# Kernel optimization log

Hardware: AMD Instinct MI355X
Metric: run time of the kernel (lower is better)

## Reference

```python
import jax, jax.numpy as jnp
import numpy as np

# Model dims (match init_kwargs)
D_MODEL = 512
NUM_EXPERTS = 8
TOP_K = 2
FFN_MULT = 2
HIDDEN = FFN_MULT * D_MODEL
BATCH, SEQ = 4, 2048


def setup_inputs() -> dict:
    key = jax.random.key(0)
    k_x, k_g, k_bg, k_w1, k_w3, k_w2 = jax.random.split(key, 6)
    sd = 1.0 / np.sqrt(D_MODEL).astype(np.float32)
    sh = 1.0 / np.sqrt(HIDDEN).astype(np.float32)
    return {
        "x": jax.random.normal(k_x, (BATCH, SEQ, D_MODEL), dtype=jnp.float32),
        # gate: nn.Linear(d_model, num_experts) with bias
        "Wg": jax.random.normal(k_g, (D_MODEL, NUM_EXPERTS), dtype=jnp.float32) * sd,
        "bg": jax.random.normal(k_bg, (NUM_EXPERTS,), dtype=jnp.float32) * 0.01,
        # stacked per-expert SwiGLU FFN params (no bias, LLaMA-style)
        "W1": jax.random.normal(k_w1, (NUM_EXPERTS, D_MODEL, HIDDEN), dtype=jnp.float32) * sd,
        "W3": jax.random.normal(k_w3, (NUM_EXPERTS, D_MODEL, HIDDEN), dtype=jnp.float32) * sd,
        "W2": jax.random.normal(k_w2, (NUM_EXPERTS, HIDDEN, D_MODEL), dtype=jnp.float32) * sh,
    }


def reference(x, Wg, bg, W1, W3, W2):
    B, S, D = x.shape
    E = Wg.shape[1]
    xt = x.reshape(-1, D)                        # [T, D], T = B*S
    T = xt.shape[0]

    # Router: top-k over experts, softmax over the k selected logits
    logits = xt @ Wg + bg                        # [T, E]
    top_vals, top_idx = jax.lax.top_k(logits, TOP_K)  # [T, K]
    top_probs = jax.nn.softmax(top_vals, axis=-1)     # [T, K]

    # Dense per-(token, expert) combine weight; zero where expert not selected.
    # top-k indices are distinct per token so scatter-add == scatter-set.
    gate_w = jnp.zeros((T, E), dtype=xt.dtype).at[
        jnp.arange(T)[:, None], top_idx
    ].add(top_probs)                              # [T, E]

    # Loop over experts (fixed, small), accumulate weighted expert outputs.
    def body(y, expert):
        w1, w3, w2, g = expert                   # g: [T]
        h = jax.nn.silu(xt @ w1) * (xt @ w3)     # [T, H]
        return y + g[:, None] * (h @ w2), None

    y0 = jnp.zeros_like(xt)
    y, _ = jax.lax.scan(body, y0, (W1, W3, W2, gate_w.T))
    return y.reshape(B, S, D)
```

## Files before the change

### kernel.cpp

```cpp
#include <hip/hip_runtime.h>
#include <hip/hip_bf16.h>

#define TOKENS 8192
#define DM 512
#define NE 8
#define HID 1024
#define NSLOT (TOKENS * 2)
#define NB 32

#define BM 128
#define BN 64
#define BK 64
#define MAXTILE 136

typedef __bf16 bf16x8 __attribute__((ext_vector_type(8)));
typedef float floatx4 __attribute__((ext_vector_type(4)));
typedef unsigned short u16x8 __attribute__((ext_vector_type(8)));

__device__ __forceinline__ unsigned short f2bf(float f) {
    union { float f; unsigned u; } c; c.f = f;
    unsigned u = c.u;
    u += 0x7fffu + ((u >> 16) & 1u);
    return (unsigned short)(u >> 16);
}

__device__ __forceinline__ void load16_lds(const void* g, void* l) {
    __builtin_amdgcn_global_load_lds(
        (const __attribute__((address_space(1))) unsigned int*)g,
        (__attribute__((address_space(3))) unsigned int*)l, 16, 0, 0);
}

__global__ void init_kernel(float* __restrict__ y) {
    const size_t n4 = (size_t)TOKENS * DM / 4;
    float4* y4 = (float4*)y;
    for (size_t i = (size_t)blockIdx.x * blockDim.x + threadIdx.x; i < n4;
         i += (size_t)gridDim.x * blockDim.x)
        y4[i] = make_float4(0.f, 0.f, 0.f, 0.f);
}

__global__ void cvt_transpose_kernel(const float* __restrict__ src, unsigned short* __restrict__ dst,
                                     int K, int N) {
    __shared__ float tile[32][33];
    const int tk = K >> 5, tn = N >> 5;
    int b = blockIdx.x;
    int e = b / (tk * tn);
    int rem = b % (tk * tn);
    int kt = rem / tn, nt = rem % tn;
    int tx = threadIdx.x & 31, ty = threadIdx.x >> 5;
    const float* s = src + ((size_t)e * K + kt * 32) * N + nt * 32;
    #pragma unroll
    for (int i = 0; i < 32; i += 8)
        tile[ty + i][tx] = s[(size_t)(ty + i) * N + tx];
    __syncthreads();
    unsigned short* d = dst + ((size_t)e * N + nt * 32) * K + kt * 32;
    #pragma unroll
    for (int i = 0; i < 32; i += 8)
        d[(size_t)(ty + i) * K + tx] = f2bf(tile[tx][ty + i]);
}

__global__ void router_kernel(const float* __restrict__ x, const float* __restrict__ Wg,
                              const float* __restrict__ bg,
                              int* __restrict__ top_idx, float* __restrict__ top_p,
                              unsigned short* __restrict__ xb) {
    int lane = threadIdx.x & 63, wave = threadIdx.x >> 6;
    int t = blockIdx.x * 4 + wave;
    float acc[NE];
    #pragma unroll
    for (int e = 0; e < NE; e++) acc[e] = 0.f;
    const float* xr = x + (size_t)t * DM;
    unsigned short* xbr = xb + (size_t)t * DM;
    #pragma unroll
    for (int j = 0; j < 8; j++) {
        int d = lane + j * 64;
        float xv = xr[d];
        xbr[d] = f2bf(xv);
        const float4* wr = (const float4*)(Wg + (size_t)d * NE);
        float4 w0 = wr[0], w1 = wr[1];
        acc[0] += xv * w0.x; acc[1] += xv * w0.y; acc[2] += xv * w0.z; acc[3] += xv * w0.w;
        acc[4] += xv * w1.x; acc[5] += xv * w1.y; acc[6] += xv * w1.z; acc[7] += xv * w1.w;
    }
    #pragma unroll
    for (int e = 0; e < NE; e++) {
        float v = acc[e];
        #pragma unroll
        for (int off = 32; off > 0; off >>= 1) v += __shfl_down(v, off, 64);
        acc[e] = v;
    }
    if (lane == 0) {
        float best = -1e30f, second = -1e30f;
        int bi = 0, si = 0;
        #pragma unroll
        for (int e = 0; e < NE; e++) {
            float v = acc[e] + bg[e];
            if (v > best) { second = best; si = bi; best = v; bi = e; }
            else if (v > second) { second = v; si = e; }
        }
        float ex = __expf(second - best);
        float inv = 1.f / (1.f + ex);
        top_idx[t * 2] = bi;  top_idx[t * 2 + 1] = si;
        top_p[t * 2] = inv;   top_p[t * 2 + 1] = ex * inv;
    }
}

__global__ void hist_kernel(const int* __restrict__ top_idx, int* __restrict__ block_hist) {
    __shared__ int h[NE];
    int b = blockIdx.x, tid = threadIdx.x;
    if (tid < NE) h[tid] = 0;
    __syncthreads();
    int t = b * 256 + tid;
    atomicAdd(&h[top_idx[t * 2]], 1);
    atomicAdd(&h[top_idx[t * 2 + 1]], 1);
    __syncthreads();
    if (tid < NE) block_hist[b * NE + tid] = h[tid];
}

__global__ void prefix_kernel(const int* __restrict__ block_hist, int* __restrict__ counts,
                              int* __restrict__ offsets, int* __restrict__ bases) {
    int e = threadIdx.x;
    if (e < NE) {
        int run = 0;
        for (int b = 0; b < NB; b++) { bases[b * NE + e] = run; run += block_hist[b * NE + e]; }
        counts[e] = run;
    }
    __syncthreads();
    if (e == 0) {
        int s = 0;
        for (int ee = 0; ee < NE; ee++) { offsets[ee] = s; s += counts[ee]; }
    }
    __syncthreads();
    if (e < NE) {
        int off = offsets[e];
        for (int b = 0; b < NB; b++) bases[b * NE + e] += off;
    }
}

__global__ void build_kernel(const int* __restrict__ top_idx, const float* __restrict__ top_p,
                             const int* __restrict__ bases,
                             int* __restrict__ rows, float* __restrict__ gates,
                             int* __restrict__ slot_of) {
    __shared__ int cur[NE];
    int b = blockIdx.x, tid = threadIdx.x;
    if (tid < NE) cur[tid] = bases[b * NE + tid];
    __syncthreads();
    int t = b * 256 + tid;
    #pragma unroll
    for (int k = 0; k < 2; k++) {
        int e = top_idx[t * 2 + k];
        int slot = atomicAdd(&cur[e], 1);
        rows[slot] = t;
        gates[slot] = top_p[t * 2 + k];
        slot_of[t * 2 + k] = slot;
    }
}

__device__ __forceinline__ bool tile_lookup(const int* counts, const int* offsets, int gy,
                                            int& e, int& mt, int& cnt, int& off) {
    int bacc = 0;
    #pragma unroll
    for (int ee = 0; ee < NE; ee++) {
        int c = counts[ee];
        int ntl = (c + BM - 1) >> 7;
        if (gy < bacc + ntl) { e = ee; mt = gy - bacc; cnt = c; off = offsets[ee]; return true; }
        bacc += ntl;
    }
    return false;
}

__global__ __launch_bounds__(256) void gemm1_kernel(
    const unsigned short* __restrict__ xb,
    const unsigned short* __restrict__ w1t,
    const unsigned short* __restrict__ w3t,
    unsigned short* __restrict__ Hb,
    const int* __restrict__ rows, const int* __restrict__ counts,
    const int* __restrict__ offsets) {
    const int nt = blockIdx.x;
    int e, mt, cnt, off;
    if (!tile_lookup(counts, offsets, blockIdx.y, e, mt, cnt, off)) return;

    __shared__ unsigned short As[2][BM * BK];
    __shared__ unsigned short B1s[2][BN * BK];
    __shared__ unsigned short B3s[2][BN * BK];

    const int tid = threadIdx.x;
    const int lane = tid & 63, wave = tid >> 6;
    const int lrow8 = lane >> 3;
    const int lchunk = (lane & 7) ^ lrow8;

    const unsigned short* a_g[4];
    #pragma unroll
    for (int i = 0; i < 4; i++) {
        int r = (wave * 4 + i) * 8 + lrow8;
        int gr = mt * BM + r;
        int tok = rows[off + (gr < cnt ? gr : 0)];
        a_g[i] = xb + (size_t)tok * DM + lchunk * 8;
    }
    const unsigned short* b1_g[2]; const unsigned short* b3_g[2];
    #pragma unroll
    for (int i = 0; i < 2; i++) {
        int r = (wave * 2 + i) * 8 + lrow8;
        b1_g[i] = w1t + ((size_t)e * HID + nt * BN + r) * DM + lchunk * 8;
        b3_g[i] = w3t + ((size_t)e * HID + nt * BN + r) * DM + lchunk * 8;
    }

    const int l15 = lane & 15, quad = lane >> 4;
    const int sw = l15 & 7;

    floatx4 acc1[2][4], acc3[2][4];
    #pragma unroll
    for (int i = 0; i < 2; i++)
        #pragma unroll
        for (int j = 0; j < 4; j++) {
            acc1[i][j] = (floatx4){0.f, 0.f, 0.f, 0.f};
            acc3[i][j] = (floatx4){0.f, 0.f, 0.f, 0.f};
        }

    auto stage = [&](int k0, int b) {
        #pragma unroll
        for (int i = 0; i < 4; i++) load16_lds(a_g[i] + k0, &As[b][(wave * 4 + i) * 512]);
        #pragma unroll
        for (int i = 0; i < 2; i++) {
            load16_lds(b1_g[i] + k0, &B1s[b][(wave * 2 + i) * 512]);
            load16_lds(b3_g[i] + k0, &B3s[b][(wave * 2 + i) * 512]);
        }
    };
    auto compute = [&](int b) {
        #pragma unroll
        for (int kk = 0; kk < 2; kk++) {
            const int qc = kk * 4 + quad;
            const int ch = (qc ^ sw) << 3;
            bf16x8 af[2], b1f[4], b3f[4];
            #pragma unroll
            for (int mi = 0; mi < 2; mi++)
                af[mi] = *(const bf16x8*)(&As[b][(wave * 32 + mi * 16 + l15) * 64 + ch]);
            #pragma unroll
            for (int ni = 0; ni < 4; ni++) {
                b1f[ni] = *(const bf16x8*)(&B1s[b][(ni * 16 + l15) * 64 + ch]);
                b3f[ni] = *(const bf16x8*)(&B3s[b][(ni * 16 + l15) * 64 + ch]);
            }
            #pragma unroll
            for (int mi = 0; mi < 2; mi++)
                #pragma unroll
                for (int ni = 0; ni < 4; ni++) {
                    acc1[mi][ni] = __builtin_amdgcn_mfma_f32_16x16x32_bf16(af[mi], b1f[ni], acc1[mi][ni], 0, 0, 0);
                    acc3[mi][ni] = __builtin_amdgcn_mfma_f32_16x16x32_bf16(af[mi], b3f[ni], acc3[mi][ni], 0, 0, 0);
                }
        }
    };

    const int NI = DM / BK;
    stage(0, 0);
    #pragma unroll
    for (int i = 0; i < NI; i += 2) {
        __syncthreads();
        if (i + 1 < NI) stage((i + 1) * BK, 1);
        compute(0);
        __syncthreads();
        if (i + 2 < NI) stage((i + 2) * BK, 0);
        compute(1);
    }
    #pragma unroll
    for (int mi = 0; mi < 2; mi++) {
        #pragma unroll
        for (int r = 0; r < 4; r++) {
            int mloc = wave * 32 + mi * 16 + quad * 4 + r;
            int gi = mt * BM + mloc;
            if (gi < cnt) {
                size_t rowbase = (size_t)(off + gi) * HID + nt * BN;
                #pragma unroll
                for (int ni = 0; ni < 4; ni++) {
                    float z1 = acc1[mi][ni][r];
                    float z3 = acc3[mi][ni][r];
                    float h = (z1 / (1.f + __expf(-z1))) * z3;
                    Hb[rowbase + ni * 16 + l15] = f2bf(h);
                }
            }
        }
    }
}

__global__ __launch_bounds__(256) void gemm2_kernel(
    const unsigned short* __restrict__ Hb,
    const unsigned short* __restrict__ w2t,
    float* __restrict__ P,
    float* __restrict__ y,
    const int* __restrict__ rows, const float* __restrict__ gates,
    const int* __restrict__ counts, const int* __restrict__ offsets) {
    const int nt = blockIdx.x;
    int e, mt, cnt, off;
    if (!tile_lookup(counts, offsets, blockIdx.y, e, mt, cnt, off)) return;

    __shared__ unsigned short As[2][BM * BK];
    __shared__ unsigned short Bs[2][BN * BK];

    const int tid = threadIdx.x;
    const int lane = tid & 63, wave = tid >> 6;
    const int lrow8 = lane >> 3;
    const int lchunk = (lane & 7) ^ lrow8;

    const unsigned short* a_g[4];
    #pragma unroll
    for (int i = 0; i < 4; i++) {
        int r = (wave * 4 + i) * 8 + lrow8;
        int sl = off + mt * BM + r;
        if (sl >= NSLOT) sl = NSLOT - 1;
        a_g[i] = Hb + (size_t)sl * HID + lchunk * 8;
    }
    const unsigned short* b_g[2];
    #pragma unroll
    for (int i = 0; i < 2; i++) {
        int r = (wave * 2 + i) * 8 + lrow8;
        b_g[i] = w2t + ((size_t)e * DM + nt * BN + r) * HID + lchunk * 8;
    }

    const int l15 = lane & 15, quad = lane >> 4;
    const int sw = l15 & 7;

    floatx4 acc[2][4];
    #pragma unroll
    for (int i = 0; i < 2; i++)
        #pragma unroll
        for (int j = 0; j < 4; j++) acc[i][j] = (floatx4){0.f, 0.f, 0.f, 0.f};

    auto stage = [&](int k0, int b) {
        #pragma unroll
        for (int i = 0; i < 4; i++) load16_lds(a_g[i] + k0, &As[b][(wave * 4 + i) * 512]);
        #pragma unroll
        for (int i = 0; i < 2; i++) load16_lds(b_g[i] + k0, &Bs[b][(wave * 2 + i) * 512]);
    };
    auto compute = [&](int b) {
        #pragma unroll
        for (int kk = 0; kk < 2; kk++) {
            const int qc = kk * 4 + quad;
            const int ch = (qc ^ sw) << 3;
            bf16x8 af[2], bf[4];
            #pragma unroll
            for (int mi = 0; mi < 2; mi++)
                af[mi] = *(const bf16x8*)(&As[b][(wave * 32 + mi * 16 + l15) * 64 + ch]);
            #pragma unroll
            for (int ni = 0; ni < 4; ni++)
                bf[ni] = *(const bf16x8*)(&Bs[b][(ni * 16 + l15) * 64 + ch]);
            #pragma unroll
            for (int mi = 0; mi < 2; mi++)
                #pragma unroll
                for (int ni = 0; ni < 4; ni++)
                    acc[mi][ni] = __builtin_amdgcn_mfma_f32_16x16x32_bf16(af[mi], bf[ni], acc[mi][ni], 0, 0, 0);
        }
    };

    const int NI = HID / BK;
    stage(0, 0);
    #pragma unroll
    for (int i = 0; i < NI; i += 2) {
        __syncthreads();
        if (i + 1 < NI) stage((i + 1) * BK, 1);
        compute(0);
        __syncthreads();
        if (i + 2 < NI) stage((i + 2) * BK, 0);
        compute(1);
    }
    const bool direct = (P == nullptr);
    #pragma unroll
    for (int mi = 0; mi < 2; mi++) {
        #pragma unroll
        for (int r = 0; r < 4; r++) {
            int mloc = wave * 32 + mi * 16 + quad * 4 + r;
            int gi = mt * BM + mloc;
            if (gi < cnt) {
                int slot = off + gi;
                float g = gates[slot];
                #pragma unroll
                for (int ni = 0; ni < 4; ni++) {
                    int col = nt * BN + ni * 16 + l15;
                    float v = g * acc[mi][ni][r];
                    if (direct) {
                        int tokr = rows[slot];
                        atomicAdd(&y[(size_t)tokr * DM + col], v);
                    } else {
                        P[(size_t)slot * DM + col] = v;
                    }
                }
            }
        }
    }
}

__global__ void combine_kernel(const float* __restrict__ P, const int* __restrict__ slot_of,
                               float* __restrict__ y) {
    int i = blockIdx.x * blockDim.x + threadIdx.x;
    int t = i / (DM / 4);
    int c4 = i % (DM / 4);
    int s0 = slot_of[t * 2], s1 = slot_of[t * 2 + 1];
    float4 a = ((const float4*)P)[(size_t)s0 * (DM / 4) + c4];
    float4 b = ((const float4*)P)[(size_t)s1 * (DM / 4) + c4];
    float4 o;
    o.x = a.x + b.x;
    o.y = a.y + b.y;
    o.z = a.z + b.z;
    o.w = a.w + b.w;
    ((float4*)y)[i] = o;
}

extern "C" void kernel_launch(void* const* d_in, const int* in_sizes, int n_in,
                              void* d_out, int out_size, void* d_ws, size_t ws_size,
                              hipStream_t stream) {
    (void)in_sizes; (void)n_in; (void)out_size;
    const float* x  = (const float*)d_in[0];
    const float* Wg = (const float*)d_in[1];
    const float* bg = (const float*)d_in[2];
    const float* W1 = (const float*)d_in[3];
    const float* W3 = (const float*)d_in[4];
    const float* W2 = (const float*)d_in[5];
    float* y = (float*)d_out;

    char* p = (char*)d_ws;
    auto carve = [&](size_t bytes) -> char* {
        char* r = p;
        p += (bytes + 255) & ~(size_t)255;
        return r;
    };
    unsigned short* xb   = (unsigned short*)carve((size_t)TOKENS * DM * 2);
    unsigned short* w1t  = (unsigned short*)carve((size_t)NE * DM * HID * 2);
    unsigned short* w3t  = (unsigned short*)carve((size_t)NE * DM * HID * 2);
    unsigned short* w2t  = (unsigned short*)carve((size_t)NE * HID * DM * 2);
    unsigned short* Hb   = (unsigned short*)carve((size_t)NSLOT * HID * 2);
    int*   rows    = (int*)carve(NSLOT * 4);
    float* gates   = (float*)carve(NSLOT * 4);
    int*   slot_of = (int*)carve(NSLOT * 4);
    int*   tidx    = (int*)carve((size_t)TOKENS * 2 * 4);
    float* tp      = (float*)carve((size_t)TOKENS * 2 * 4);
    int*   counts  = (int*)carve(256);
    int*   offsets = (int*)carve(256);
    int*   bhist   = (int*)carve((size_t)NB * NE * 4);
    int*   bases   = (int*)carve((size_t)NB * NE * 4);
    size_t base_need = (size_t)(p - (char*)d_ws);
    const size_t PBYTES = (size_t)NSLOT * DM * 4;
    float* P = nullptr;
    if (ws_size >= base_need + PBYTES) P = (float*)carve(PBYTES);

    if (P == nullptr)
        init_kernel<<<dim3(1024), dim3(256), 0, stream>>>(y);
    router_kernel<<<dim3(TOKENS / 4), dim3(256), 0, stream>>>(x, Wg, bg, tidx, tp, xb);
    cvt_transpose_kernel<<<dim3(NE * (DM / 32) * (HID / 32)), dim3(256), 0, stream>>>(W1, w1t, DM, HID);
    cvt_transpose_kernel<<<dim3(NE * (DM / 32) * (HID / 32)), dim3(256), 0, stream>>>(W3, w3t, DM, HID);
    cvt_transpose_kernel<<<dim3(NE * (HID / 32) * (DM / 32)), dim3(256), 0, stream>>>(W2, w2t, HID, DM);
    hist_kernel<<<dim3(NB), dim3(256), 0, stream>>>(tidx, bhist);
    prefix_kernel<<<dim3(1), dim3(64), 0, stream>>>(bhist, counts, offsets, bases);
    build_kernel<<<dim3(NB), dim3(256), 0, stream>>>(tidx, tp, bases, rows, gates, slot_of);
    gemm1_kernel<<<dim3(HID / BN, MAXTILE, 1), dim3(256), 0, stream>>>(xb, w1t, w3t, Hb, rows, counts, offsets);
    gemm2_kernel<<<dim3(DM / BN, MAXTILE, 1), dim3(256), 0, stream>>>(Hb, w2t, P, y, rows, gates, counts, offsets);
    if (P != nullptr)
        combine_kernel<<<dim3((TOKENS * DM / 4) / 256), dim3(256), 0, stream>>>(P, slot_of, y);
}
```

Measured before the change: 241.1 us.

## Enlarge GEMM tiles to 2D wave layout, halve BK, merge weight-convert launches

Both expert GEMMs move from 1D row-split waves to a 2x2 (or 4x2) wave grid with 64x64 per-wave sub-tiles. This uses bigger block tiles (128x128 for gemm1, 256x128 with 512 threads for gemm2) and BK 32 with a new LDS swizzle. The goal is more operand reuse per LDS load and fewer global loads per FLOP. The three weight convert-transpose launches are merged into one 2D-grid launch to cut launch overhead. Larger accumulator arrays raise register pressure, and fewer, larger tiles mean more padding waste on partial expert tiles.

```diff
diff --git a/kernel.cpp b/kernel.cpp
--- a/kernel.cpp
+++ b/kernel.cpp
@@ -8,10 +8,13 @@
 #define NSLOT (TOKENS * 2)
 #define NB 32
 
-#define BM 128
-#define BN 64
-#define BK 64
-#define MAXTILE 136
+#define BK 32
+#define BM1 128
+#define BN1 128
+#define MAXTILE1 136
+#define BM2 256
+#define BN2 128
+#define MAXTILE2 72
 
 typedef __bf16 bf16x8 __attribute__((ext_vector_type(8)));
 typedef float floatx4 __attribute__((ext_vector_type(4)));
@@ -38,9 +41,15 @@
         y4[i] = make_float4(0.f, 0.f, 0.f, 0.f);
 }
 
-__global__ void cvt_transpose_kernel(const float* __restrict__ src, unsigned short* __restrict__ dst,
-                                     int K, int N) {
+__global__ void cvt_transpose_kernel(const float* __restrict__ W1, const float* __restrict__ W3,
+                                     const float* __restrict__ W2,
+                                     unsigned short* __restrict__ w1t, unsigned short* __restrict__ w3t,
+                                     unsigned short* __restrict__ w2t) {
     __shared__ float tile[32][33];
+    const float* src; unsigned short* dst; int K, N;
+    if (blockIdx.y == 0)      { src = W1; dst = w1t; K = DM;  N = HID; }
+    else if (blockIdx.y == 1) { src = W3; dst = w3t; K = DM;  N = HID; }
+    else                      { src = W2; dst = w2t; K = HID; N = DM;  }
     const int tk = K >> 5, tn = N >> 5;
     int b = blockIdx.x;
     int e = b / (tk * tn);
@@ -154,19 +163,19 @@
 }
 
 __device__ __forceinline__ bool tile_lookup(const int* counts, const int* offsets, int gy,
-                                            int& e, int& mt, int& cnt, int& off) {
+                                            int bmshift, int& e, int& mt, int& cnt, int& off) {
     int bacc = 0;
     #pragma unroll
     for (int ee = 0; ee < NE; ee++) {
         int c = counts[ee];
-        int ntl = (c + BM - 1) >> 7;
+        int ntl = (c + (1 << bmshift) - 1) >> bmshift;
         if (gy < bacc + ntl) { e = ee; mt = gy - bacc; cnt = c; off = offsets[ee]; return true; }
         bacc += ntl;
     }
     return false;
 }
 
-__global__ __launch_bounds__(256) void gemm1_kernel(
+__global__ __launch_bounds__(256, 2) void gemm1_kernel(
     const unsigned short* __restrict__ xb,
     const unsigned short* __restrict__ w1t,
     const unsigned short* __restrict__ w3t,
@@ -175,39 +184,40 @@
     const int* __restrict__ offsets) {
     const int nt = blockIdx.x;
     int e, mt, cnt, off;
-    if (!tile_lookup(counts, offsets, blockIdx.y, e, mt, cnt, off)) return;
-
-    __shared__ unsigned short As[2][BM * BK];
-    __shared__ unsigned short B1s[2][BN * BK];
-    __shared__ unsigned short B3s[2][BN * BK];
+    if (!tile_lookup(counts, offsets, blockIdx.y, 7, e, mt, cnt, off)) return;
+
+    __shared__ unsigned short As[2][BM1 * BK];
+    __shared__ unsigned short B1s[2][BN1 * BK];
+    __shared__ unsigned short B3s[2][BN1 * BK];
 
     const int tid = threadIdx.x;
     const int lane = tid & 63, wave = tid >> 6;
-    const int lrow8 = lane >> 3;
-    const int lchunk = (lane & 7) ^ lrow8;
-
-    const unsigned short* a_g[4];
-    #pragma unroll
-    for (int i = 0; i < 4; i++) {
-        int r = (wave * 4 + i) * 8 + lrow8;
-        int gr = mt * BM + r;
+    const int lr = lane >> 2;
+    const int lc = (lane & 3) ^ ((lane >> 3) & 3);
+
+    const unsigned short* a_g[2];
+    #pragma unroll
+    for (int i = 0; i < 2; i++) {
+        int r = wave * 32 + i * 16 + lr;
+        int gr = mt * BM1 + r;
         int tok = rows[off + (gr < cnt ? gr : 0)];
-        a_g[i] = xb + (size_t)tok * DM + lchunk * 8;
+        a_g[i] = xb + (size_t)tok * DM + lc * 8;
     }
     const unsigned short* b1_g[2]; const unsigned short* b3_g[2];
     #pragma unroll
     for (int i = 0; i < 2; i++) {
-        int r = (wave * 2 + i) * 8 + lrow8;
-        b1_g[i] = w1t + ((size_t)e * HID + nt * BN + r) * DM + lchunk * 8;
-        b3_g[i] = w3t + ((size_t)e * HID + nt * BN + r) * DM + lchunk * 8;
+        int r = wave * 32 + i * 16 + lr;
+        b1_g[i] = w1t + ((size_t)e * HID + nt * BN1 + r) * DM + lc * 8;
+        b3_g[i] = w3t + ((size_t)e * HID + nt * BN1 + r) * DM + lc * 8;
     }
 
     const int l15 = lane & 15, quad = lane >> 4;
-    const int sw = l15 & 7;
-
-    floatx4 acc1[2][4], acc3[2][4];
-    #pragma unroll
-    for (int i = 0; i < 2; i++)
+    const int rsw = (l15 >> 1) & 3;
+    const int m0 = (wave >> 1) * 64, n0 = (wave & 1) * 64;
+
+    floatx4 acc1[4][4], acc3[4][4];
+    #pragma unroll
+    for (int i = 0; i < 4; i++)
         #pragma unroll
         for (int j = 0; j < 4; j++) {
             acc1[i][j] = (floatx4){0.f, 0.f, 0.f, 0.f};
@@ -216,40 +226,34 @@
 
     auto stage = [&](int k0, int b) {
         #pragma unroll
-        for (int i = 0; i < 4; i++) load16_lds(a_g[i] + k0, &As[b][(wave * 4 + i) * 512]);
-        #pragma unroll
         for (int i = 0; i < 2; i++) {
-            load16_lds(b1_g[i] + k0, &B1s[b][(wave * 2 + i) * 512]);
-            load16_lds(b3_g[i] + k0, &B3s[b][(wave * 2 + i) * 512]);
+            load16_lds(a_g[i] + k0, &As[b][(wave * 32 + i * 16) * BK]);
+            load16_lds(b1_g[i] + k0, &B1s[b][(wave * 32 + i * 16) * BK]);
+            load16_lds(b3_g[i] + k0, &B3s[b][(wave * 32 + i * 16) * BK]);
         }
     };
     auto compute = [&](int b) {
-        #pragma unroll
-        for (int kk = 0; kk < 2; kk++) {
-            const int qc = kk * 4 + quad;
-            const int ch = (qc ^ sw) << 3;
-            bf16x8 af[2], b1f[4], b3f[4];
-            #pragma unroll
-            for (int mi = 0; mi < 2; mi++)
-                af[mi] = *(const bf16x8*)(&As[b][(wave * 32 + mi * 16 + l15) * 64 + ch]);
+        const int ch = ((quad ^ rsw) << 3);
+        bf16x8 af[4], b1f[4], b3f[4];
+        #pragma unroll
+        for (int mi = 0; mi < 4; mi++)
+            af[mi] = *(const bf16x8*)(&As[b][(m0 + mi * 16 + l15) * BK + ch]);
+        #pragma unroll
+        for (int ni = 0; ni < 4; ni++) {
+            b1f[ni] = *(const bf16x8*)(&B1s[b][(n0 + ni * 16 + l15) * BK + ch]);
+            b3f[ni] = *(const bf16x8*)(&B3s[b][(n0 + ni * 16 + l15) * BK + ch]);
+        }
+        #pragma unroll
+        for (int mi = 0; mi < 4; mi++)
             #pragma unroll
             for (int ni = 0; ni < 4; ni++) {
-                b1f[ni] = *(const bf16x8*)(&B1s[b][(ni * 16 + l15) * 64 + ch]);
-                b3f[ni] = *(const bf16x8*)(&B3s[b][(ni * 16 + l15) * 64 + ch]);
+                acc1[mi][ni] = __builtin_amdgcn_mfma_f32_16x16x32_bf16(af[mi], b1f[ni], acc1[mi][ni], 0, 0, 0);
+                acc3[mi][ni] = __builtin_amdgcn_mfma_f32_16x16x32_bf16(af[mi], b3f[ni], acc3[mi][ni], 0, 0, 0);
             }
-            #pragma unroll
-            for (int mi = 0; mi < 2; mi++)
-                #pragma unroll
-                for (int ni = 0; ni < 4; ni++) {
-                    acc1[mi][ni] = __builtin_amdgcn_mfma_f32_16x16x32_bf16(af[mi], b1f[ni], acc1[mi][ni], 0, 0, 0);
-                    acc3[mi][ni] = __builtin_amdgcn_mfma_f32_16x16x32_bf16(af[mi], b3f[ni], acc3[mi][ni], 0, 0, 0);
-                }
-        }
     };
 
     const int NI = DM / BK;
     stage(0, 0);
-    #pragma unroll
     for (int i = 0; i < NI; i += 2) {
         __syncthreads();
         if (i + 1 < NI) stage((i + 1) * BK, 1);
@@ -259,13 +263,13 @@
         compute(1);
     }
     #pragma unroll
-    for (int mi = 0; mi < 2; mi++) {
+    for (int mi = 0; mi < 4; mi++) {
         #pragma unroll
         for (int r = 0; r < 4; r++) {
-            int mloc = wave * 32 + mi * 16 + quad * 4 + r;
-            int gi = mt * BM + mloc;
+            int mloc = m0 + mi * 16 + quad * 4 + r;
+            int gi = mt * BM1 + mloc;
             if (gi < cnt) {
-                size_t rowbase = (size_t)(off + gi) * HID + nt * BN;
+                size_t rowbase = (size_t)(off + gi) * HID + nt * BN1 + n0;
                 #pragma unroll
                 for (int ni = 0; ni < 4; ni++) {
                     float z1 = acc1[mi][ni][r];
@@ -278,7 +282,7 @@
     }
 }
 
-__global__ __launch_bounds__(256) void gemm2_kernel(
+__global__ __launch_bounds__(512, 4) void gemm2_kernel(
     const unsigned short* __restrict__ Hb,
     const unsigned short* __restrict__ w2t,
     float* __restrict__ P,
@@ -287,69 +291,60 @@
     const int* __restrict__ counts, const int* __restrict__ offsets) {
     const int nt = blockIdx.x;
     int e, mt, cnt, off;
-    if (!tile_lookup(counts, offsets, blockIdx.y, e, mt, cnt, off)) return;
-
-    __shared__ unsigned short As[2][BM * BK];
-    __shared__ unsigned short Bs[2][BN * BK];
+    if (!tile_lookup(counts, offsets, blockIdx.y, 8, e, mt, cnt, off)) return;
+
+    __shared__ unsigned short As[2][BM2 * BK];
+    __shared__ unsigned short Bs[2][BN2 * BK];
 
     const int tid = threadIdx.x;
     const int lane = tid & 63, wave = tid >> 6;
-    const int lrow8 = lane >> 3;
-    const int lchunk = (lane & 7) ^ lrow8;
-
-    const unsigned short* a_g[4];
-    #pragma unroll
-    for (int i = 0; i < 4; i++) {
-        int r = (wave * 4 + i) * 8 + lrow8;
-        int sl = off + mt * BM + r;
+    const int lr = lane >> 2;
+    const int lc = (lane & 3) ^ ((lane >> 3) & 3);
+
+    const unsigned short* a_g[2];
+    #pragma unroll
+    for (int i = 0; i < 2; i++) {
+        int r = wave * 32 + i * 16 + lr;
+        int sl = off + mt * BM2 + r;
         if (sl >= NSLOT) sl = NSLOT - 1;
-        a_g[i] = Hb + (size_t)sl * HID + lchunk * 8;
-    }
-    const unsigned short* b_g[2];
-    #pragma unroll
-    for (int i = 0; i < 2; i++) {
-        int r = (wave * 2 + i) * 8 + lrow8;
-        b_g[i] = w2t + ((size_t)e * DM + nt * BN + r) * HID + lchunk * 8;
-    }
+        a_g[i] = Hb + (size_t)sl * HID + lc * 8;
+    }
+    const unsigned short* b_g = w2t + ((size_t)e * DM + nt * BN2 + wave * 16 + lr) * HID + lc * 8;
 
     const int l15 = lane & 15, quad = lane >> 4;
-    const int sw = l15 & 7;
-
-    floatx4 acc[2][4];
-    #pragma unroll
-    for (int i = 0; i < 2; i++)
+    const int rsw = (l15 >> 1) & 3;
+    const int m0 = (wave >> 1) * 64, n0 = (wave & 1) * 64;
+
+    floatx4 acc[4][4];
+    #pragma unroll
+    for (int i = 0; i < 4; i++)
         #pragma unroll
         for (int j = 0; j < 4; j++) acc[i][j] = (floatx4){0.f, 0.f, 0.f, 0.f};
 
     auto stage = [&](int k0, int b) {
         #pragma unroll
-        for (int i = 0; i < 4; i++) load16_lds(a_g[i] + k0, &As[b][(wave * 4 + i) * 512]);
-        #pragma unroll
-        for (int i = 0; i < 2; i++) load16_lds(b_g[i] + k0, &Bs[b][(wave * 2 + i) * 512]);
+        for (int i = 0; i < 2; i++)
+            load16_lds(a_g[i] + k0, &As[b][(wave * 32 + i * 16) * BK]);
+        load16_lds(b_g + k0, &Bs[b][(wave * 16) * BK]);
     };
     auto compute = [&](int b) {
-        #pragma unroll
-        for (int kk = 0; kk < 2; kk++) {
-            const int qc = kk * 4 + quad;
-            const int ch = (qc ^ sw) << 3;
-            bf16x8 af[2], bf[4];
-            #pragma unroll
-            for (int mi = 0; mi < 2; mi++)
-                af[mi] = *(const bf16x8*)(&As[b][(wave * 32 + mi * 16 + l15) * 64 + ch]);
+        const int ch = ((quad ^ rsw) << 3);
+        bf16x8 af[4], bf[4];
+        #pragma unroll
+        for (int mi = 0; mi < 4; mi++)
+            af[mi] = *(const bf16x8*)(&As[b][(m0 + mi * 16 + l15) * BK + ch]);
+        #pragma unroll
+        for (int ni = 0; ni < 4; ni++)
+            bf[ni] = *(const bf16x8*)(&Bs[b][(n0 + ni * 16 + l15) * BK + ch]);
+        #pragma unroll
+        for (int mi = 0; mi < 4; mi++)
             #pragma unroll
             for (int ni = 0; ni < 4; ni++)
-                bf[ni] = *(const bf16x8*)(&Bs[b][(ni * 16 + l15) * 64 + ch]);
-            #pragma unroll
-            for (int mi = 0; mi < 2; mi++)
-                #pragma unroll
-                for (int ni = 0; ni < 4; ni++)
-                    acc[mi][ni] = __builtin_amdgcn_mfma_f32_16x16x32_bf16(af[mi], bf[ni], acc[mi][ni], 0, 0, 0);
-        }
+                acc[mi][ni] = __builtin_amdgcn_mfma_f32_16x16x32_bf16(af[mi], bf[ni], acc[mi][ni], 0, 0, 0);
     };
 
     const int NI = HID / BK;
     stage(0, 0);
-    #pragma unroll
     for (int i = 0; i < NI; i += 2) {
         __syncthreads();
         if (i + 1 < NI) stage((i + 1) * BK, 1);
@@ -360,17 +355,17 @@
     }
     const bool direct = (P == nullptr);
     #pragma unroll
-    for (int mi = 0; mi < 2; mi++) {
+    for (int mi = 0; mi < 4; mi++) {
         #pragma unroll
         for (int r = 0; r < 4; r++) {
-            int mloc = wave * 32 + mi * 16 + quad * 4 + r;
-            int gi = mt * BM + mloc;
+            int mloc = m0 + mi * 16 + quad * 4 + r;
+            int gi = mt * BM2 + mloc;
             if (gi < cnt) {
                 int slot = off + gi;
                 float g = gates[slot];
                 #pragma unroll
                 for (int ni = 0; ni < 4; ni++) {
-                    int col = nt * BN + ni * 16 + l15;
+                    int col = nt * BN2 + n0 + ni * 16 + l15;
                     float v = g * acc[mi][ni][r];
                     if (direct) {
                         int tokr = rows[slot];
@@ -440,14 +435,12 @@
     if (P == nullptr)
         init_kernel<<<dim3(1024), dim3(256), 0, stream>>>(y);
     router_kernel<<<dim3(TOKENS / 4), dim3(256), 0, stream>>>(x, Wg, bg, tidx, tp, xb);
-    cvt_transpose_kernel<<<dim3(NE * (DM / 32) * (HID / 32)), dim3(256), 0, stream>>>(W1, w1t, DM, HID);
-    cvt_transpose_kernel<<<dim3(NE * (DM / 32) * (HID / 32)), dim3(256), 0, stream>>>(W3, w3t, DM, HID);
-    cvt_transpose_kernel<<<dim3(NE * (HID / 32) * (DM / 32)), dim3(256), 0, stream>>>(W2, w2t, HID, DM);
+    cvt_transpose_kernel<<<dim3(NE * 16 * 32, 3), dim3(256), 0, stream>>>(W1, W3, W2, w1t, w3t, w2t);
     hist_kernel<<<dim3(NB), dim3(256), 0, stream>>>(tidx, bhist);
     prefix_kernel<<<dim3(1), dim3(64), 0, stream>>>(bhist, counts, offsets, bases);
     build_kernel<<<dim3(NB), dim3(256), 0, stream>>>(tidx, tp, bases, rows, gates, slot_of);
-    gemm1_kernel<<<dim3(HID / BN, MAXTILE, 1), dim3(256), 0, stream>>>(xb, w1t, w3t, Hb, rows, counts, offsets);
-    gemm2_kernel<<<dim3(DM / BN, MAXTILE, 1), dim3(256), 0, stream>>>(Hb, w2t, P, y, rows, gates, counts, offsets);
+    gemm1_kernel<<<dim3(HID / BN1, MAXTILE1), dim3(256), 0, stream>>>(xb, w1t, w3t, Hb, rows, counts, offsets);
+    gemm2_kernel<<<dim3(DM / BN2, MAXTILE2), dim3(512), 0, stream>>>(Hb, w2t, P, y, rows, gates, counts, offsets);
     if (P != nullptr)
         combine_kernel<<<dim3((TOKENS * DM / 4) / 256), dim3(256), 0, stream>>>(P, slot_of, y);
 }
```

Result: no change. 237.2 us (-1.6%).

## Merge weight transposes, store gemm2 partials as bf16 reusing w1t buffer

Applied to the files above, without the earlier changes.

The three weight convert-transpose launches become one launch with a 3-wide grid. gemm2 now always writes gate-scaled partial outputs as bf16 into a scratch buffer aliased onto the w1t workspace, which is dead after gemm1, instead of fp32 partials or atomics. The combine kernel reads bf16 pairs and sums them in fp32. This drops the atomic/init fallback and halves partial-buffer traffic, at the cost of extra bf16 rounding on each expert output before combining.

```diff
diff --git a/kernel.cpp b/kernel.cpp
--- a/kernel.cpp
+++ b/kernel.cpp
@@ -30,17 +30,15 @@
         (__attribute__((address_space(3))) unsigned int*)l, 16, 0, 0);
 }
 
-__global__ void init_kernel(float* __restrict__ y) {
-    const size_t n4 = (size_t)TOKENS * DM / 4;
-    float4* y4 = (float4*)y;
-    for (size_t i = (size_t)blockIdx.x * blockDim.x + threadIdx.x; i < n4;
-         i += (size_t)gridDim.x * blockDim.x)
-        y4[i] = make_float4(0.f, 0.f, 0.f, 0.f);
-}
-
-__global__ void cvt_transpose_kernel(const float* __restrict__ src, unsigned short* __restrict__ dst,
-                                     int K, int N) {
+__global__ void cvt_transpose_kernel(const float* __restrict__ W1, const float* __restrict__ W3,
+                                     const float* __restrict__ W2,
+                                     unsigned short* __restrict__ w1t, unsigned short* __restrict__ w3t,
+                                     unsigned short* __restrict__ w2t) {
     __shared__ float tile[32][33];
+    const float* src; unsigned short* dst; int K, N;
+    if (blockIdx.y == 0)      { src = W1; dst = w1t; K = DM;  N = HID; }
+    else if (blockIdx.y == 1) { src = W3; dst = w3t; K = DM;  N = HID; }
+    else                      { src = W2; dst = w2t; K = HID; N = DM;  }
     const int tk = K >> 5, tn = N >> 5;
     int b = blockIdx.x;
     int e = b / (tk * tn);
@@ -281,9 +279,8 @@
 __global__ __launch_bounds__(256) void gemm2_kernel(
     const unsigned short* __restrict__ Hb,
     const unsigned short* __restrict__ w2t,
-    float* __restrict__ P,
-    float* __restrict__ y,
-    const int* __restrict__ rows, const float* __restrict__ gates,
+    unsigned short* __restrict__ P,
+    const float* __restrict__ gates,
     const int* __restrict__ counts, const int* __restrict__ offsets) {
     const int nt = blockIdx.x;
     int e, mt, cnt, off;
@@ -358,7 +355,6 @@
         if (i + 2 < NI) stage((i + 2) * BK, 0);
         compute(1);
     }
-    const bool direct = (P == nullptr);
     #pragma unroll
     for (int mi = 0; mi < 2; mi++) {
         #pragma unroll
@@ -371,39 +367,41 @@
                 #pragma unroll
                 for (int ni = 0; ni < 4; ni++) {
                     int col = nt * BN + ni * 16 + l15;
-                    float v = g * acc[mi][ni][r];
-                    if (direct) {
-                        int tokr = rows[slot];
-                        atomicAdd(&y[(size_t)tokr * DM + col], v);
-                    } else {
-                        P[(size_t)slot * DM + col] = v;
-                    }
+                    P[(size_t)slot * DM + col] = f2bf(g * acc[mi][ni][r]);
                 }
             }
         }
     }
 }
 
-__global__ void combine_kernel(const float* __restrict__ P, const int* __restrict__ slot_of,
-                               float* __restrict__ y) {
+__global__ void combine_kernel(const unsigned short* __restrict__ P,
+                               const int* __restrict__ slot_of, float* __restrict__ y) {
     int i = blockIdx.x * blockDim.x + threadIdx.x;
-    int t = i / (DM / 4);
-    int c4 = i % (DM / 4);
+    int t = i / (DM / 8);
+    int c8 = i % (DM / 8);
     int s0 = slot_of[t * 2], s1 = slot_of[t * 2 + 1];
-    float4 a = ((const float4*)P)[(size_t)s0 * (DM / 4) + c4];
-    float4 b = ((const float4*)P)[(size_t)s1 * (DM / 4) + c4];
-    float4 o;
-    o.x = a.x + b.x;
-    o.y = a.y + b.y;
-    o.z = a.z + b.z;
-    o.w = a.w + b.w;
-    ((float4*)y)[i] = o;
+    uint4 a = *(const uint4*)(P + (size_t)s0 * DM + c8 * 8);
+    uint4 b = *(const uint4*)(P + (size_t)s1 * DM + c8 * 8);
+    float o[8];
+    const unsigned* aw = (const unsigned*)&a;
+    const unsigned* bw = (const unsigned*)&b;
+    #pragma unroll
+    for (int j = 0; j < 4; j++) {
+        union { unsigned u; float f; } al, ah, bl, bh;
+        al.u = aw[j] << 16; ah.u = aw[j] & 0xffff0000u;
+        bl.u = bw[j] << 16; bh.u = bw[j] & 0xffff0000u;
+        o[j * 2]     = al.f + bl.f;
+        o[j * 2 + 1] = ah.f + bh.f;
+    }
+    float4* yo = (float4*)(y + (size_t)t * DM + c8 * 8);
+    yo[0] = make_float4(o[0], o[1], o[2], o[3]);
+    yo[1] = make_float4(o[4], o[5], o[6], o[7]);
 }
 
 extern "C" void kernel_launch(void* const* d_in, const int* in_sizes, int n_in,
                               void* d_out, int out_size, void* d_ws, size_t ws_size,
                               hipStream_t stream) {
-    (void)in_sizes; (void)n_in; (void)out_size;
+    (void)in_sizes; (void)n_in; (void)out_size; (void)ws_size;
     const float* x  = (const float*)d_in[0];
     const float* Wg = (const float*)d_in[1];
     const float* bg = (const float*)d_in[2];
@@ -432,22 +430,14 @@
     int*   offsets = (int*)carve(256);
     int*   bhist   = (int*)carve((size_t)NB * NE * 4);
     int*   bases   = (int*)carve((size_t)NB * NE * 4);
-    size_t base_need = (size_t)(p - (char*)d_ws);
-    const size_t PBYTES = (size_t)NSLOT * DM * 4;
-    float* P = nullptr;
-    if (ws_size >= base_need + PBYTES) P = (float*)carve(PBYTES);
-
-    if (P == nullptr)
-        init_kernel<<<dim3(1024), dim3(256), 0, stream>>>(y);
+    unsigned short* P = w1t;
+
     router_kernel<<<dim3(TOKENS / 4), dim3(256), 0, stream>>>(x, Wg, bg, tidx, tp, xb);
-    cvt_transpose_kernel<<<dim3(NE * (DM / 32) * (HID / 32)), dim3(256), 0, stream>>>(W1, w1t, DM, HID);
-    cvt_transpose_kernel<<<dim3(NE * (DM / 32) * (HID / 32)), dim3(256), 0, stream>>>(W3, w3t, DM, HID);
-    cvt_transpose_kernel<<<dim3(NE * (HID / 32) * (DM / 32)), dim3(256), 0, stream>>>(W2, w2t, HID, DM);
+    cvt_transpose_kernel<<<dim3(NE * 16 * 32, 3), dim3(256), 0, stream>>>(W1, W3, W2, w1t, w3t, w2t);
     hist_kernel<<<dim3(NB), dim3(256), 0, stream>>>(tidx, bhist);
     prefix_kernel<<<dim3(1), dim3(64), 0, stream>>>(bhist, counts, offsets, bases);
     build_kernel<<<dim3(NB), dim3(256), 0, stream>>>(tidx, tp, bases, rows, gates, slot_of);
-    gemm1_kernel<<<dim3(HID / BN, MAXTILE, 1), dim3(256), 0, stream>>>(xb, w1t, w3t, Hb, rows, counts, offsets);
-    gemm2_kernel<<<dim3(DM / BN, MAXTILE, 1), dim3(256), 0, stream>>>(Hb, w2t, P, y, rows, gates, counts, offsets);
-    if (P != nullptr)
-        combine_kernel<<<dim3((TOKENS * DM / 4) / 256), dim3(256), 0, stream>>>(P, slot_of, y);
-}
+    gemm1_kernel<<<dim3(HID / BN, MAXTILE), dim3(256), 0, stream>>>(xb, w1t, w3t, Hb, rows, counts, offsets);
+    gemm2_kernel<<<dim3(DM / BN, MAXTILE), dim3(256), 0, stream>>>(Hb, w2t, P, gates, counts, offsets);
+    combine_kernel<<<dim3((TOKENS * DM / 8) / 256), dim3(256), 0, stream>>>(P, slot_of, y);
+}
```

New measurement: 232.2 us. 3.7% less time.
